# Performance work log

Measured on AMD Instinct MI355X. Metric: run time of the kernel, lower is better.

The kernel has to match this reference:

```python
import jax, jax.numpy as jnp
import numpy as np

B, N, F_IN, F_OUT = 8, 2048, 128, 64
ALPHA = 0.2  # LeakyReLU negative slope
NEG_BIG = -9e15


def setup_inputs() -> dict:
    key = jax.random.key(0)
    k1, k2, k3, k4 = jax.random.split(key, 4)
    x = jax.random.normal(k1, (B, N, F_IN), dtype=jnp.float32)
    adj = jax.random.randint(k2, (B, N, N), 0, 2, dtype=jnp.int32)
    # xavier-uniform-ish init scale for faithfulness (gain=1.414)
    w_lim = 1.414 * np.sqrt(6.0 / (F_IN + F_OUT))
    a_lim = 1.414 * np.sqrt(6.0 / (2 * F_OUT + 1))
    weight = jax.random.uniform(k3, (F_IN, F_OUT), minval=-w_lim, maxval=w_lim, dtype=jnp.float32)
    weight2 = jax.random.uniform(k4, (2 * F_OUT, 1), minval=-a_lim, maxval=a_lim, dtype=jnp.float32)
    return {"x": x, "adj": adj, "weight": weight, "weight2": weight2}


def reference(x, adj, weight, weight2):
    # Linear projection: [B, N, F_out]
    wh = jnp.einsum("bnf,fo->bno", x, weight)
    # Additive GAT decomposition of concat-score:
    # e_ij = leakyrelu(a1 . Wh_i + a2 . Wh_j)  == original concat @ weight2
    a1 = weight2[:F_OUT, 0]   # [F_out]
    a2 = weight2[F_OUT:, 0]   # [F_out]
    s1 = wh @ a1              # [B, N]
    s2 = wh @ a2              # [B, N]
    e = s1[:, :, None] + s2[:, None, :]          # [B, N, N]
    e = jnp.where(e > 0, e, ALPHA * e)            # LeakyReLU
    e = jnp.where(adj > 0, e, NEG_BIG)            # mask non-edges
    attention = jax.nn.softmax(e, axis=2)         # [B, N, N]
    # dropout is identity in eval mode (training=False)
    out = jnp.einsum("bij,bjo->bio", attention, wh)  # [B, N, F_out]
    return jax.nn.elu(out)
```

## Files before the change

### kernel.cpp

```cpp
#include <hip/hip_runtime.h>
#include <cstdint>
#include <cstddef>

#define B_    8
#define N_    2048
#define FIN   128
#define FOUT  64
#define ALPHA 0.2f
#define LOG2E 1.4426950408889634f

typedef __attribute__((ext_vector_type(8))) _Float16 half8;
typedef __attribute__((ext_vector_type(4))) _Float16 half4;
typedef __attribute__((ext_vector_type(4))) float float4v;

__global__ __launch_bounds__(256, 2) void k1_wh(
    const float* __restrict__ x, const float* __restrict__ W,
    const float* __restrict__ w2, const int* __restrict__ adj,
    _Float16* __restrict__ whT, float* __restrict__ s1, float* __restrict__ s2,
    unsigned long long* __restrict__ maskp)
{
    __shared__ __attribute__((aligned(16))) _Float16 xth[32][136];
    __shared__ __attribute__((aligned(16))) _Float16 xtl[32][136];
    __shared__ float s1p[4][32];
    __shared__ float s2p[4][32];

    int t = threadIdx.x, lane = t & 63, w = t >> 6;
    int b = blockIdx.x >> 6;
    int r0 = (blockIdx.x & 63) << 5;
    const float* xb = x + ((size_t)b * N_ + r0) * FIN;

    #pragma unroll
    for (int j = 0; j < 4; ++j) {
        int idx = t + j * 256;
        int row = idx >> 5;
        int k0 = (idx & 31) * 4;
        float4 v = ((const float4*)xb)[idx];
        float vv[4] = {v.x, v.y, v.z, v.w};
        half4 h, l;
        #pragma unroll
        for (int e = 0; e < 4; ++e) {
            _Float16 hi = (_Float16)vv[e];
            h[e] = hi;
            l[e] = (_Float16)(vv[e] - (float)hi);
        }
        *(half4*)&xth[row][k0] = h;
        *(half4*)&xtl[row][k0] = l;
    }
    __syncthreads();

    int l15 = lane & 15, quad = lane >> 4;
    int f0 = w * 16;

    half8 bh[4], bl[4];
    const float* wcol = W + (f0 + l15);
    #pragma unroll
    for (int c = 0; c < 4; ++c) {
        #pragma unroll
        for (int e = 0; e < 8; ++e) {
            float v = wcol[(size_t)(c * 32 + quad * 8 + e) * FOUT];
            _Float16 hi = (_Float16)v;
            bh[c][e] = hi;
            bl[c][e] = (_Float16)(v - (float)hi);
        }
    }
    float a1f = w2[f0 + l15], a2f = w2[FOUT + f0 + l15];

    #pragma unroll
    for (int rt = 0; rt < 2; ++rt) {
        float4v acc = {0.f, 0.f, 0.f, 0.f};
        #pragma unroll
        for (int c = 0; c < 4; ++c) {
            half8 ah = *(const half8*)&xth[rt * 16 + l15][c * 32 + quad * 8];
            half8 al = *(const half8*)&xtl[rt * 16 + l15][c * 32 + quad * 8];
            acc = __builtin_amdgcn_mfma_f32_16x16x32_f16(ah, bh[c], acc, 0, 0, 0);
            acc = __builtin_amdgcn_mfma_f32_16x16x32_f16(ah, bl[c], acc, 0, 0, 0);
            acc = __builtin_amdgcn_mfma_f32_16x16x32_f16(al, bh[c], acc, 0, 0, 0);
        }
        half4 hv;
        #pragma unroll
        for (int reg = 0; reg < 4; ++reg) hv[reg] = (_Float16)acc[reg];
        *(half4*)(whT + ((size_t)b * FOUT + f0 + l15) * N_ + r0 + rt * 16 + quad * 4) = hv;

        #pragma unroll
        for (int reg = 0; reg < 4; ++reg) {
            float v1 = acc[reg] * a1f;
            float v2 = acc[reg] * a2f;
            #pragma unroll
            for (int m = 1; m <= 8; m <<= 1) {
                v1 += __shfl_xor(v1, m);
                v2 += __shfl_xor(v2, m);
            }
            if (l15 == 0) {
                s1p[w][rt * 16 + quad * 4 + reg] = v1;
                s2p[w][rt * 16 + quad * 4 + reg] = v2;
            }
        }
    }
    __syncthreads();
    if (t < 32) {
        float v = s1p[0][t] + s1p[1][t] + s1p[2][t] + s1p[3][t];
        s1[(size_t)b * N_ + r0 + t] = v;
    } else if (t < 64) {
        int r = t - 32;
        float v = s2p[0][r] + s2p[1][r] + s2p[2][r] + s2p[3][r];
        s2[(size_t)b * N_ + r0 + r] = v;
    }

    size_t growbase = (size_t)b * N_ + r0 + (size_t)w * 8;
    #pragma unroll 1
    for (int r = 0; r < 8; ++r) {
        const int* rp = adj + (growbase + r) * N_ + lane;
        unsigned long long* orow = maskp + (growbase + r) * 32;
        int a[32];
        #pragma unroll
        for (int it = 0; it < 32; ++it) a[it] = rp[it * 64];
        #pragma unroll
        for (int it = 0; it < 32; ++it) {
            unsigned long long m = __ballot(a[it] > 0);
            if (lane == 0) orow[it] = m;
        }
    }
}

__global__ __launch_bounds__(256, 4) void k2_attn(
    const unsigned* __restrict__ mask32, const _Float16* __restrict__ whT,
    const float* __restrict__ s1, const float* __restrict__ s2,
    float* __restrict__ out)
{
    __shared__ __attribute__((aligned(16))) _Float16 pT[2][16][264];
    __shared__ float lL[16];
    __shared__ float smaxL[4];

    int t = threadIdx.x, lane = t & 63, w = t >> 6;
    int b = blockIdx.x >> 7;
    int i0 = (blockIdx.x & 127) << 4;

    const float4* s2v = (const float4*)(s2 + (size_t)b * N_);
    float4 ua_ = s2v[t], ub_ = s2v[t + 256];
    float vm = fmaxf(fmaxf(fmaxf(ua_.x, ua_.y), fmaxf(ua_.z, ua_.w)),
                     fmaxf(fmaxf(ub_.x, ub_.y), fmaxf(ub_.z, ub_.w)));
    #pragma unroll
    for (int m = 32; m >= 1; m >>= 1) vm = fmaxf(vm, __shfl_xor(vm, m));
    if (lane == 0) smaxL[w] = vm;
    __syncthreads();
    float s2max = fmaxf(fmaxf(smaxL[0], smaxL[1]), fmaxf(smaxL[2], smaxL[3]));

    int l15 = lane & 15, quad = lane >> 4;
    int f0 = w * 16;
    int shn = (lane & 7) * 4;

    float c1[4], c2[4], lacc[4];
    #pragma unroll
    for (int rr = 0; rr < 4; ++rr) {
        float sv = s1[(size_t)b * N_ + i0 + w * 4 + rr];
        float mm = sv + s2max;
        float mh = fmaxf(mm, ALPHA * mm);
        c1[rr] = (sv - mh) * LOG2E;
        c2[rr] = (ALPHA * sv - mh) * LOG2E;
        lacc[rr] = 0.f;
    }

    const unsigned* mB = mask32 + ((size_t)b * N_ + i0 + w * 4) * 64 + (lane >> 3);
    const float* s2L = s2 + (size_t)b * N_ + lane * 4;
    const _Float16* wB = whT + ((size_t)b * FOUT + f0 + l15) * N_ + quad * 8;

    float4v acc = {0.f, 0.f, 0.f, 0.f};

    unsigned mb0[4], mb1[4];
    float4 sv0, sv1;
    half8 bfr[8];

#define LOADMS(cc, MB, SV) do {                                              \
        _Pragma("unroll")                                                    \
        for (int rr_ = 0; rr_ < 4; ++rr_)                                    \
            MB[rr_] = mB[(size_t)rr_ * 64 + (cc) * 8];                       \
        SV = *(const float4*)(s2L + (cc) * 256);                             \
    } while (0)

#define LOADBF(cc) do {                                                      \
        const _Float16* wp_ = wB + (cc) * 256;                               \
        _Pragma("unroll")                                                    \
        for (int kk_ = 0; kk_ < 8; ++kk_)                                    \
            bfr[kk_] = *(const half8*)(wp_ + kk_ * 32);                      \
    } while (0)

#define PCOMP(MB, SV, PB) do {                                               \
        float u_[4]  = {SV.x * LOG2E, SV.y * LOG2E, SV.z * LOG2E, SV.w * LOG2E}; \
        float ua2_[4] = {u_[0] * ALPHA, u_[1] * ALPHA, u_[2] * ALPHA, u_[3] * ALPHA}; \
        _Pragma("unroll")                                                    \
        for (int rr_ = 0; rr_ < 4; ++rr_) {                                  \
            unsigned mbits_ = (MB[rr_] >> shn) & 0xFu;                       \
            half4 pf_;                                                       \
            float ls_ = 0.f;                                                 \
            _Pragma("unroll")                                                \
            for (int e_ = 0; e_ < 4; ++e_) {                                 \
                float tt_ = fmaxf(c1[rr_] + u_[e_], c2[rr_] + ua2_[e_]);     \
                float p_ = __builtin_amdgcn_exp2f(tt_);                      \
                p_ = (mbits_ & (1u << e_)) ? p_ : 0.f;                       \
                ls_ += p_;                                                   \
                pf_[e_] = (_Float16)p_;                                      \
            }                                                                \
            lacc[rr_] += ls_;                                                \
            *(half4*)&pT[PB][w * 4 + rr_][lane * 4] = pf_;                   \
        }                                                                    \
    } while (0)

#define MFMA8(PB) do {                                                       \
        _Pragma("unroll")                                                    \
        for (int kk_ = 0; kk_ < 8; ++kk_) {                                  \
            half8 af_ = *(const half8*)&pT[PB][l15][kk_ * 32 + quad * 8];    \
            acc = __builtin_amdgcn_mfma_f32_16x16x32_f16(af_, bfr[kk_], acc, 0, 0, 0); \
        }                                                                    \
    } while (0)

    LOADMS(0, mb0, sv0);

    #pragma unroll 1
    for (int c = 0; c < 8; c += 2) {
        LOADBF(c);
        LOADMS(c + 1, mb1, sv1);
        PCOMP(mb0, sv0, 0);
        __syncthreads();
        MFMA8(0);
        LOADBF(c + 1);
        if (c < 6) LOADMS(c + 2, mb0, sv0);
        PCOMP(mb1, sv1, 1);
        if (c == 6) {
            #pragma unroll
            for (int rr = 0; rr < 4; ++rr) {
                float v = lacc[rr];
                #pragma unroll
                for (int m = 32; m >= 1; m >>= 1) v += __shfl_xor(v, m);
                if (lane == 0) lL[w * 4 + rr] = v;
            }
        }
        __syncthreads();
        MFMA8(1);
    }
#undef LOADMS
#undef LOADBF
#undef PCOMP
#undef MFMA8

    #pragma unroll
    for (int reg = 0; reg < 4; ++reg) {
        int row = quad * 4 + reg;
        float val = acc[reg] / lL[row];
        val = (val > 0.f) ? val : (__expf(val) - 1.f);
        out[((size_t)b * N_ + i0 + row) * FOUT + f0 + l15] = val;
    }
}

extern "C" void kernel_launch(void* const* d_in, const int* in_sizes, int n_in,
                              void* d_out, int out_size, void* d_ws, size_t ws_size,
                              hipStream_t stream) {
    const float* x   = (const float*)d_in[0];
    const int*   adj = (const int*)d_in[1];
    const float* W   = (const float*)d_in[2];
    const float* w2  = (const float*)d_in[3];
    float* out = (float*)d_out;

    char* ws = (char*)d_ws;
    _Float16* whT = (_Float16*)ws;
    float* s1  = (float*)(ws + 2097152);
    float* s2  = (float*)(ws + 2097152 + 65536);
    unsigned long long* maskp =
        (unsigned long long*)(ws + 2097152 + 131072);

    k1_wh<<<(B_ * N_) / 32, 256, 0, stream>>>(x, W, w2, adj, whT, s1, s2, maskp);
    k2_attn<<<(B_ * N_) / 16, 256, 0, stream>>>((const unsigned*)maskp, whT, s1, s2, out);
}
```

Measured before the change: 241.2 us.

## Fuse projection and attention kernels with per-batch grid barrier and shared-memory mask

Merges the Wh/score projection kernel and the attention kernel into one launch, with each block handling 16 rows. Each block packs its own adjacency rows into a shared-memory bitmask instead of writing it to global memory and reading it back. A per-batch atomic spin barrier makes the whole batch's whT and s2 visible before attention starts, and a memset resets the counters each call. This removes the global mask round trip and one launch, but it depends on all 1024 blocks being co-resident to avoid deadlock, and it adds the memset plus spin waiting.

```diff
diff --git a/kernel.cpp b/kernel.cpp
--- a/kernel.cpp
+++ b/kernel.cpp
@@ -13,24 +13,31 @@
 typedef __attribute__((ext_vector_type(4))) _Float16 half4;
 typedef __attribute__((ext_vector_type(4))) float float4v;
 
-__global__ __launch_bounds__(256, 2) void k1_wh(
-    const float* __restrict__ x, const float* __restrict__ W,
-    const float* __restrict__ w2, const int* __restrict__ adj,
+__global__ __launch_bounds__(256, 4) void kfused(
+    const float* __restrict__ x, const int* __restrict__ adj,
+    const float* __restrict__ W, const float* __restrict__ w2,
     _Float16* __restrict__ whT, float* __restrict__ s1, float* __restrict__ s2,
-    unsigned long long* __restrict__ maskp)
+    unsigned* __restrict__ bar, float* __restrict__ out)
 {
-    __shared__ __attribute__((aligned(16))) _Float16 xth[32][136];
-    __shared__ __attribute__((aligned(16))) _Float16 xtl[32][136];
-    __shared__ float s1p[4][32];
-    __shared__ float s2p[4][32];
+    __shared__ __attribute__((aligned(16))) _Float16 xth[16][136];
+    __shared__ __attribute__((aligned(16))) _Float16 xtl[16][136];
+    __shared__ float s1p[4][16];
+    __shared__ float s2p[4][16];
+    __shared__ __attribute__((aligned(16))) unsigned long long maskS[16][32];
+    __shared__ __attribute__((aligned(16))) _Float16 pT[2][16][264];
+    __shared__ float lL[16];
+    __shared__ float smaxL[4];
 
     int t = threadIdx.x, lane = t & 63, w = t >> 6;
-    int b = blockIdx.x >> 6;
-    int r0 = (blockIdx.x & 63) << 5;
-    const float* xb = x + ((size_t)b * N_ + r0) * FIN;
-
-    #pragma unroll
-    for (int j = 0; j < 4; ++j) {
+    int blk = blockIdx.x;
+    int b = blk >> 7;
+    int i0 = (blk & 127) << 4;
+    int l15 = lane & 15, quad = lane >> 4;
+    int f0 = w * 16;
+
+    const float* xb = x + ((size_t)b * N_ + i0) * FIN;
+    #pragma unroll
+    for (int j = 0; j < 2; ++j) {
         int idx = t + j * 256;
         int row = idx >> 5;
         int k0 = (idx & 31) * 4;
@@ -48,92 +55,83 @@
     }
     __syncthreads();
 
-    int l15 = lane & 15, quad = lane >> 4;
-    int f0 = w * 16;
-
-    half8 bh[4], bl[4];
-    const float* wcol = W + (f0 + l15);
-    #pragma unroll
-    for (int c = 0; c < 4; ++c) {
-        #pragma unroll
-        for (int e = 0; e < 8; ++e) {
-            float v = wcol[(size_t)(c * 32 + quad * 8 + e) * FOUT];
-            _Float16 hi = (_Float16)v;
-            bh[c][e] = hi;
-            bl[c][e] = (_Float16)(v - (float)hi);
-        }
-    }
-    float a1f = w2[f0 + l15], a2f = w2[FOUT + f0 + l15];
-
-    #pragma unroll
-    for (int rt = 0; rt < 2; ++rt) {
-        float4v acc = {0.f, 0.f, 0.f, 0.f};
+    {
+        half8 bh[4], bl[4];
+        const float* wcol = W + (f0 + l15);
         #pragma unroll
         for (int c = 0; c < 4; ++c) {
-            half8 ah = *(const half8*)&xth[rt * 16 + l15][c * 32 + quad * 8];
-            half8 al = *(const half8*)&xtl[rt * 16 + l15][c * 32 + quad * 8];
-            acc = __builtin_amdgcn_mfma_f32_16x16x32_f16(ah, bh[c], acc, 0, 0, 0);
-            acc = __builtin_amdgcn_mfma_f32_16x16x32_f16(ah, bl[c], acc, 0, 0, 0);
-            acc = __builtin_amdgcn_mfma_f32_16x16x32_f16(al, bh[c], acc, 0, 0, 0);
+            #pragma unroll
+            for (int e = 0; e < 8; ++e) {
+                float v = wcol[(size_t)(c * 32 + quad * 8 + e) * FOUT];
+                _Float16 hi = (_Float16)v;
+                bh[c][e] = hi;
+                bl[c][e] = (_Float16)(v - (float)hi);
+            }
+        }
+        float a1f = w2[f0 + l15], a2f = w2[FOUT + f0 + l15];
+
+        float4v acc1 = {0.f, 0.f, 0.f, 0.f};
+        #pragma unroll
+        for (int c = 0; c < 4; ++c) {
+            half8 ah = *(const half8*)&xth[l15][c * 32 + quad * 8];
+            half8 al = *(const half8*)&xtl[l15][c * 32 + quad * 8];
+            acc1 = __builtin_amdgcn_mfma_f32_16x16x32_f16(ah, bh[c], acc1, 0, 0, 0);
+            acc1 = __builtin_amdgcn_mfma_f32_16x16x32_f16(ah, bl[c], acc1, 0, 0, 0);
+            acc1 = __builtin_amdgcn_mfma_f32_16x16x32_f16(al, bh[c], acc1, 0, 0, 0);
         }
         half4 hv;
         #pragma unroll
-        for (int reg = 0; reg < 4; ++reg) hv[reg] = (_Float16)acc[reg];
-        *(half4*)(whT + ((size_t)b * FOUT + f0 + l15) * N_ + r0 + rt * 16 + quad * 4) = hv;
+        for (int reg = 0; reg < 4; ++reg) hv[reg] = (_Float16)acc1[reg];
+        *(half4*)(whT + ((size_t)b * FOUT + f0 + l15) * N_ + i0 + quad * 4) = hv;
 
         #pragma unroll
         for (int reg = 0; reg < 4; ++reg) {
-            float v1 = acc[reg] * a1f;
-            float v2 = acc[reg] * a2f;
+            float v1 = acc1[reg] * a1f;
+            float v2 = acc1[reg] * a2f;
             #pragma unroll
             for (int m = 1; m <= 8; m <<= 1) {
                 v1 += __shfl_xor(v1, m);
                 v2 += __shfl_xor(v2, m);
             }
             if (l15 == 0) {
-                s1p[w][rt * 16 + quad * 4 + reg] = v1;
-                s2p[w][rt * 16 + quad * 4 + reg] = v2;
-            }
-        }
-    }
-    __syncthreads();
-    if (t < 32) {
-        float v = s1p[0][t] + s1p[1][t] + s1p[2][t] + s1p[3][t];
-        s1[(size_t)b * N_ + r0 + t] = v;
-    } else if (t < 64) {
-        int r = t - 32;
-        float v = s2p[0][r] + s2p[1][r] + s2p[2][r] + s2p[3][r];
-        s2[(size_t)b * N_ + r0 + r] = v;
-    }
-
-    size_t growbase = (size_t)b * N_ + r0 + (size_t)w * 8;
-    #pragma unroll 1
-    for (int r = 0; r < 8; ++r) {
-        const int* rp = adj + (growbase + r) * N_ + lane;
-        unsigned long long* orow = maskp + (growbase + r) * 32;
-        int a[32];
-        #pragma unroll
-        for (int it = 0; it < 32; ++it) a[it] = rp[it * 64];
-        #pragma unroll
-        for (int it = 0; it < 32; ++it) {
-            unsigned long long m = __ballot(a[it] > 0);
-            if (lane == 0) orow[it] = m;
-        }
-    }
-}
-
-__global__ __launch_bounds__(256, 4) void k2_attn(
-    const unsigned* __restrict__ mask32, const _Float16* __restrict__ whT,
-    const float* __restrict__ s1, const float* __restrict__ s2,
-    float* __restrict__ out)
-{
-    __shared__ __attribute__((aligned(16))) _Float16 pT[2][16][264];
-    __shared__ float lL[16];
-    __shared__ float smaxL[4];
-
-    int t = threadIdx.x, lane = t & 63, w = t >> 6;
-    int b = blockIdx.x >> 7;
-    int i0 = (blockIdx.x & 127) << 4;
+                s1p[w][quad * 4 + reg] = v1;
+                s2p[w][quad * 4 + reg] = v2;
+            }
+        }
+    }
+    __syncthreads();
+    if (t < 16) {
+        s1[(size_t)b * N_ + i0 + t] = s1p[0][t] + s1p[1][t] + s1p[2][t] + s1p[3][t];
+    } else if (t < 32) {
+        int r = t - 16;
+        s2[(size_t)b * N_ + i0 + r] = s2p[0][r] + s2p[1][r] + s2p[2][r] + s2p[3][r];
+    }
+
+    {
+        size_t growbase = (size_t)b * N_ + i0 + (size_t)w * 4;
+        #pragma unroll 1
+        for (int r = 0; r < 4; ++r) {
+            const int* rp = adj + (growbase + r) * N_ + lane;
+            int a[32];
+            #pragma unroll
+            for (int it = 0; it < 32; ++it) a[it] = rp[it * 64];
+            #pragma unroll
+            for (int it = 0; it < 32; ++it) {
+                unsigned long long m = __ballot(a[it] > 0);
+                if (lane == 0) maskS[w * 4 + r][it] = m;
+            }
+        }
+    }
+
+    __syncthreads();
+    if (t == 0) {
+        __hip_atomic_fetch_add(&bar[b], 1u, __ATOMIC_ACQ_REL,
+                               __HIP_MEMORY_SCOPE_AGENT);
+        while (__hip_atomic_load(&bar[b], __ATOMIC_ACQUIRE,
+                                 __HIP_MEMORY_SCOPE_AGENT) < 128u)
+            __builtin_amdgcn_s_sleep(2);
+    }
+    __syncthreads();
 
     const float4* s2v = (const float4*)(s2 + (size_t)b * N_);
     float4 ua_ = s2v[t], ub_ = s2v[t + 256];
@@ -145,9 +143,8 @@
     __syncthreads();
     float s2max = fmaxf(fmaxf(smaxL[0], smaxL[1]), fmaxf(smaxL[2], smaxL[3]));
 
-    int l15 = lane & 15, quad = lane >> 4;
-    int f0 = w * 16;
     int shn = (lane & 7) * 4;
+    int oct = lane >> 3;
 
     float c1[4], c2[4], lacc[4];
     #pragma unroll
@@ -160,12 +157,11 @@
         lacc[rr] = 0.f;
     }
 
-    const unsigned* mB = mask32 + ((size_t)b * N_ + i0 + w * 4) * 64 + (lane >> 3);
+    const unsigned* mSL = (const unsigned*)&maskS[w * 4][0];
     const float* s2L = s2 + (size_t)b * N_ + lane * 4;
     const _Float16* wB = whT + ((size_t)b * FOUT + f0 + l15) * N_ + quad * 8;
 
     float4v acc = {0.f, 0.f, 0.f, 0.f};
-
     unsigned mb0[4], mb1[4];
     float4 sv0, sv1;
     half8 bfr[8];
@@ -173,7 +169,7 @@
 #define LOADMS(cc, MB, SV) do {                                              \
         _Pragma("unroll")                                                    \
         for (int rr_ = 0; rr_ < 4; ++rr_)                                    \
-            MB[rr_] = mB[(size_t)rr_ * 64 + (cc) * 8];                       \
+            MB[rr_] = mSL[rr_ * 64 + (cc) * 8 + oct];                        \
         SV = *(const float4*)(s2L + (cc) * 256);                             \
     } while (0)
 
@@ -264,9 +260,8 @@
     _Float16* whT = (_Float16*)ws;
     float* s1  = (float*)(ws + 2097152);
     float* s2  = (float*)(ws + 2097152 + 65536);
-    unsigned long long* maskp =
-        (unsigned long long*)(ws + 2097152 + 131072);
-
-    k1_wh<<<(B_ * N_) / 32, 256, 0, stream>>>(x, W, w2, adj, whT, s1, s2, maskp);
-    k2_attn<<<(B_ * N_) / 16, 256, 0, stream>>>((const unsigned*)maskp, whT, s1, s2, out);
+    unsigned* bar = (unsigned*)(ws + 2097152 + 131072);
+
+    hipMemsetAsync(bar, 0, 8 * sizeof(unsigned), stream);
+    kfused<<<(B_ * N_) / 16, 256, 0, stream>>>(x, adj, W, w2, whT, s1, s2, bar, out);
 }
```

Result: slower. 309.1 us (+28.1%).

## Split attention K dimension across waves, computing probabilities in MFMA A-registers

Applied to the files above, without the earlier changes.

The attention kernel now gives each wave a quarter of the neighbour (j) range and all 64 output features, instead of a quarter of the features over the full j range. Each lane computes its probability fragment directly in MFMA A-operand layout, which removes the shared-memory staging of probabilities and the per-chunk block barriers. Partial accumulators and row sums are reduced across the four waves through shared memory at the end. This trades the old software-pipelined prefetching for a simple unpipelined loop and adds a cross-wave reduction.

```diff
diff --git a/kernel.cpp b/kernel.cpp
--- a/kernel.cpp
+++ b/kernel.cpp
@@ -127,127 +127,99 @@
     const float* __restrict__ s1, const float* __restrict__ s2,
     float* __restrict__ out)
 {
-    __shared__ __attribute__((aligned(16))) _Float16 pT[2][16][264];
-    __shared__ float lL[16];
-    __shared__ float smaxL[4];
+    __shared__ float accL[4][64][17];
+    __shared__ float laccL[4][16];
 
     int t = threadIdx.x, lane = t & 63, w = t >> 6;
     int b = blockIdx.x >> 7;
     int i0 = (blockIdx.x & 127) << 4;
+    int l15 = lane & 15, quad = lane >> 4;
 
     const float4* s2v = (const float4*)(s2 + (size_t)b * N_);
-    float4 ua_ = s2v[t], ub_ = s2v[t + 256];
-    float vm = fmaxf(fmaxf(fmaxf(ua_.x, ua_.y), fmaxf(ua_.z, ua_.w)),
-                     fmaxf(fmaxf(ub_.x, ub_.y), fmaxf(ub_.z, ub_.w)));
+    float vm = -1e30f;
+    #pragma unroll
+    for (int j = 0; j < 8; ++j) {
+        float4 v = s2v[lane + j * 64];
+        vm = fmaxf(vm, fmaxf(fmaxf(v.x, v.y), fmaxf(v.z, v.w)));
+    }
     #pragma unroll
     for (int m = 32; m >= 1; m >>= 1) vm = fmaxf(vm, __shfl_xor(vm, m));
-    if (lane == 0) smaxL[w] = vm;
+    float s2max = vm;
+
+    float sv = s1[(size_t)b * N_ + i0 + l15];
+    float mm = sv + s2max;
+    float mh = fmaxf(mm, ALPHA * mm);
+    float c1 = (sv - mh) * LOG2E;
+    float c2 = (ALPHA * sv - mh) * LOG2E;
+    float lacc = 0.f;
+
+    const unsigned* mRow = mask32 + ((size_t)b * N_ + i0 + l15) * 64 + w * 16;
+    const float* s2base = s2 + (size_t)b * N_ + w * 512 + quad * 8;
+    const _Float16* wBb = whT + ((size_t)b * FOUT + l15) * N_ + w * 512 + quad * 8;
+
+    float4v acc0 = {0.f,0.f,0.f,0.f}, acc1 = {0.f,0.f,0.f,0.f};
+    float4v acc2 = {0.f,0.f,0.f,0.f}, acc3 = {0.f,0.f,0.f,0.f};
+
+    #pragma unroll 1
+    for (int ks = 0; ks < 16; ++ks) {
+        unsigned mw = mRow[ks];
+        unsigned mby = (mw >> (quad * 8)) & 0xFFu;
+        const float* sp = s2base + ks * 32;
+        float4 sa = *(const float4*)sp;
+        float4 sb = *(const float4*)(sp + 4);
+        const _Float16* wp = wBb + ks * 32;
+        half8 b0 = *(const half8*)(wp);
+        half8 b1 = *(const half8*)(wp + (size_t)16 * N_);
+        half8 b2 = *(const half8*)(wp + (size_t)32 * N_);
+        half8 b3 = *(const half8*)(wp + (size_t)48 * N_);
+
+        float ss[8] = {sa.x, sa.y, sa.z, sa.w, sb.x, sb.y, sb.z, sb.w};
+        half8 pa;
+        float ls = 0.f;
+        #pragma unroll
+        for (int e = 0; e < 8; ++e) {
+            float u = ss[e] * LOG2E;
+            float tt = fmaxf(c1 + u, c2 + u * ALPHA);
+#if __has_builtin(__builtin_amdgcn_exp2f)
+            float p = __builtin_amdgcn_exp2f(tt);
+#else
+            float p = exp2f(tt);
+#endif
+            p = (mby & (1u << e)) ? p : 0.f;
+            ls += p;
+            pa[e] = (_Float16)p;
+        }
+        lacc += ls;
+
+        acc0 = __builtin_amdgcn_mfma_f32_16x16x32_f16(pa, b0, acc0, 0, 0, 0);
+        acc1 = __builtin_amdgcn_mfma_f32_16x16x32_f16(pa, b1, acc1, 0, 0, 0);
+        acc2 = __builtin_amdgcn_mfma_f32_16x16x32_f16(pa, b2, acc2, 0, 0, 0);
+        acc3 = __builtin_amdgcn_mfma_f32_16x16x32_f16(pa, b3, acc3, 0, 0, 0);
+    }
+
+    lacc += __shfl_xor(lacc, 16);
+    lacc += __shfl_xor(lacc, 32);
+    if (lane < 16) laccL[w][lane] = lacc;
+    #pragma unroll
+    for (int reg = 0; reg < 4; ++reg) {
+        accL[w][lane][reg]      = acc0[reg];
+        accL[w][lane][4 + reg]  = acc1[reg];
+        accL[w][lane][8 + reg]  = acc2[reg];
+        accL[w][lane][12 + reg] = acc3[reg];
+    }
     __syncthreads();
-    float s2max = fmaxf(fmaxf(smaxL[0], smaxL[1]), fmaxf(smaxL[2], smaxL[3]));
-
-    int l15 = lane & 15, quad = lane >> 4;
-    int f0 = w * 16;
-    int shn = (lane & 7) * 4;
-
-    float c1[4], c2[4], lacc[4];
-    #pragma unroll
-    for (int rr = 0; rr < 4; ++rr) {
-        float sv = s1[(size_t)b * N_ + i0 + w * 4 + rr];
-        float mm = sv + s2max;
-        float mh = fmaxf(mm, ALPHA * mm);
-        c1[rr] = (sv - mh) * LOG2E;
-        c2[rr] = (ALPHA * sv - mh) * LOG2E;
-        lacc[rr] = 0.f;
-    }
-
-    const unsigned* mB = mask32 + ((size_t)b * N_ + i0 + w * 4) * 64 + (lane >> 3);
-    const float* s2L = s2 + (size_t)b * N_ + lane * 4;
-    const _Float16* wB = whT + ((size_t)b * FOUT + f0 + l15) * N_ + quad * 8;
-
-    float4v acc = {0.f, 0.f, 0.f, 0.f};
-
-    unsigned mb0[4], mb1[4];
-    float4 sv0, sv1;
-    half8 bfr[8];
-
-#define LOADMS(cc, MB, SV) do {                                              \
-        _Pragma("unroll")                                                    \
-        for (int rr_ = 0; rr_ < 4; ++rr_)                                    \
-            MB[rr_] = mB[(size_t)rr_ * 64 + (cc) * 8];                       \
-        SV = *(const float4*)(s2L + (cc) * 256);                             \
-    } while (0)
-
-#define LOADBF(cc) do {                                                      \
-        const _Float16* wp_ = wB + (cc) * 256;                               \
-        _Pragma("unroll")                                                    \
-        for (int kk_ = 0; kk_ < 8; ++kk_)                                    \
-            bfr[kk_] = *(const half8*)(wp_ + kk_ * 32);                      \
-    } while (0)
-
-#define PCOMP(MB, SV, PB) do {                                               \
-        float u_[4]  = {SV.x * LOG2E, SV.y * LOG2E, SV.z * LOG2E, SV.w * LOG2E}; \
-        float ua2_[4] = {u_[0] * ALPHA, u_[1] * ALPHA, u_[2] * ALPHA, u_[3] * ALPHA}; \
-        _Pragma("unroll")                                                    \
-        for (int rr_ = 0; rr_ < 4; ++rr_) {                                  \
-            unsigned mbits_ = (MB[rr_] >> shn) & 0xFu;                       \
-            half4 pf_;                                                       \
-            float ls_ = 0.f;                                                 \
-            _Pragma("unroll")                                                \
-            for (int e_ = 0; e_ < 4; ++e_) {                                 \
-                float tt_ = fmaxf(c1[rr_] + u_[e_], c2[rr_] + ua2_[e_]);     \
-                float p_ = __builtin_amdgcn_exp2f(tt_);                      \
-                p_ = (mbits_ & (1u << e_)) ? p_ : 0.f;                       \
-                ls_ += p_;                                                   \
-                pf_[e_] = (_Float16)p_;                                      \
-            }                                                                \
-            lacc[rr_] += ls_;                                                \
-            *(half4*)&pT[PB][w * 4 + rr_][lane * 4] = pf_;                   \
-        }                                                                    \
-    } while (0)
-
-#define MFMA8(PB) do {                                                       \
-        _Pragma("unroll")                                                    \
-        for (int kk_ = 0; kk_ < 8; ++kk_) {                                  \
-            half8 af_ = *(const half8*)&pT[PB][l15][kk_ * 32 + quad * 8];    \
-            acc = __builtin_amdgcn_mfma_f32_16x16x32_f16(af_, bfr[kk_], acc, 0, 0, 0); \
-        }                                                                    \
-    } while (0)
-
-    LOADMS(0, mb0, sv0);
-
-    #pragma unroll 1
-    for (int c = 0; c < 8; c += 2) {
-        LOADBF(c);
-        LOADMS(c + 1, mb1, sv1);
-        PCOMP(mb0, sv0, 0);
-        __syncthreads();
-        MFMA8(0);
-        LOADBF(c + 1);
-        if (c < 6) LOADMS(c + 2, mb0, sv0);
-        PCOMP(mb1, sv1, 1);
-        if (c == 6) {
-            #pragma unroll
-            for (int rr = 0; rr < 4; ++rr) {
-                float v = lacc[rr];
-                #pragma unroll
-                for (int m = 32; m >= 1; m >>= 1) v += __shfl_xor(v, m);
-                if (lane == 0) lL[w * 4 + rr] = v;
-            }
-        }
-        __syncthreads();
-        MFMA8(1);
-    }
-#undef LOADMS
-#undef LOADBF
-#undef PCOMP
-#undef MFMA8
 
     #pragma unroll
     for (int reg = 0; reg < 4; ++reg) {
         int row = quad * 4 + reg;
-        float val = acc[reg] / lL[row];
+        int idx = w * 4 + reg;
+        float v = accL[0][lane][idx] + accL[1][lane][idx]
+                + accL[2][lane][idx] + accL[3][lane][idx];
+        float ssum = laccL[0][row] + laccL[1][row]
+                   + laccL[2][row] + laccL[3][row];
+        float val = v / ssum;
         val = (val > 0.f) ? val : (__expf(val) - 1.f);
-        out[((size_t)b * N_ + i0 + row) * FOUT + f0 + l15] = val;
+        out[((size_t)b * N_ + i0 + row) * FOUT + w * 16 + l15] = val;
     }
 }
 
```

After: 247.8 us. 2.7% more time.
